# Kernel tuning notes

Hardware: AMD Instinct MI355X
Metric: run time of the kernel (lower is better)

Reference implementation:

```python
import jax, jax.numpy as jnp
import numpy as np

B, N, D_IN, H, D_H, D_OUT = 2, 1024, 1024, 16, 64, 1024
NEG = -1e9


def skew_relative(QE_t):
    # QE_t: [B, H, N, 2N-1] -> [B, H, N, N] via the pad/reshape skew trick
    b, h, n = QE_t.shape[0], QE_t.shape[1], QE_t.shape[2]
    x = jnp.pad(QE_t, ((0, 0), (0, 0), (0, 0), (0, 1)))          # [B,H,N,2N]
    x = x.reshape(b, h, -1)                                       # [B,H,2N^2]
    x = jnp.pad(x, ((0, 0), (0, 0), (0, n - 1)))                  # [B,H,(N+1)(2N-1)]
    x = x.reshape(b, h, n + 1, 2 * n - 1)
    return x[:, :, :n, -n:]


def setup_inputs() -> dict:
    key = jax.random.key(0)
    ks = jax.random.split(key, 8)
    x = jax.random.normal(ks[0], (B, N, D_IN), dtype=jnp.float32)
    E_rel = jax.random.normal(ks[1], (2 * N - 1, D_H), dtype=jnp.float32)
    # additive causal mask [1,1,N,N]
    causal = jnp.tril(jnp.ones((N, N), dtype=bool))
    mask = jnp.where(causal, 0.0, NEG).astype(jnp.float32)[None, None]
    s = 1.0 / np.sqrt(D_IN)
    Wq = jax.random.normal(ks[2], (D_IN, H * D_H), dtype=jnp.float32) * s
    Wk = jax.random.normal(ks[3], (D_IN, H * D_H), dtype=jnp.float32) * s
    Wv = jax.random.normal(ks[4], (D_IN, H * D_H), dtype=jnp.float32) * s
    Wo = jax.random.normal(ks[5], (H * D_H, D_OUT), dtype=jnp.float32) * (1.0 / np.sqrt(H * D_H))
    bo = jnp.zeros((D_OUT,), dtype=jnp.float32)
    return {"x": x, "E_rel": E_rel, "mask": mask, "Wq": Wq, "Wk": Wk, "Wv": Wv, "Wo": Wo, "bo": bo}


def reference(x, E_rel, mask, Wq, Wk, Wv, Wo, bo):
    b = x.shape[0]
    scale = 1.0 / np.sqrt(D_H)
    # project and split heads -> [B, H, N, d]
    Q = (x @ Wq).reshape(b, -1, H, D_H).transpose(0, 2, 1, 3)
    K = (x @ Wk).reshape(b, -1, H, D_H).transpose(0, 2, 1, 3)
    V = (x @ Wv).reshape(b, -1, H, D_H).transpose(0, 2, 1, 3)
    attn = jnp.einsum('bhnd,bhmd->bhnm', Q, K)                    # [B,H,N,N]
    QE_t = jnp.einsum('bhnd,rd->bhnr', Q, E_rel)                  # [B,H,N,2N-1]
    attn = (attn + skew_relative(QE_t)) * scale + mask
    attn = jax.nn.softmax(attn, axis=-1)
    out = jnp.einsum('bhnm,bhmd->bhnd', attn, V)                  # [B,H,N,d]
    out = out.transpose(0, 2, 1, 3).reshape(b, -1, H * D_H)
    return out @ Wo + bo  # dropout is identity at inference
```

## Files before the change

### kernel.cpp

```cpp
#include <hip/hip_runtime.h>
#include <cstdint>
#include <cstddef>

typedef __bf16 bf16;
typedef __bf16 bf16x8 __attribute__((ext_vector_type(8)));
typedef float  f32x4  __attribute__((ext_vector_type(4)));

#define MFMA16(a,b,c) __builtin_amdgcn_mfma_f32_16x16x32_bf16((a),(b),(c),0,0,0)

__device__ __forceinline__ void gload_lds16(const bf16* g, bf16* l) {
  __builtin_amdgcn_global_load_lds((__attribute__((address_space(1))) void*)(g),
                                   (__attribute__((address_space(3))) void*)(l),
                                   16, 0, 0);
}

__global__ __launch_bounds__(256) void prep_k(
    const float* __restrict__ x, const float* __restrict__ E,
    const float* __restrict__ W0, const float* __restrict__ W1,
    const float* __restrict__ W2, const float* __restrict__ W3,
    bf16* __restrict__ xb, bf16* __restrict__ Eb, bf16* __restrict__ Wt) {
  __shared__ float t[32][33];
  const int bid = blockIdx.x;
  const int tid = threadIdx.x;
  if (bid < 2176) {
    const bool isx = (bid < 2048);
    const float* src = isx ? x : E;
    bf16* dst = isx ? xb : Eb;
    const int n = isx ? (2048 * 1024) : (2047 * 64);
    const int i = (isx ? bid : (bid - 2048)) * 1024 + tid * 4;
    if (i < n) {
      float4 v = *(const float4*)(src + i);
      dst[i + 0] = (bf16)v.x;
      dst[i + 1] = (bf16)v.y;
      dst[i + 2] = (bf16)v.z;
      dst[i + 3] = (bf16)v.w;
    }
  } else {
    const int tt = bid - 2176;
    const int z = tt >> 10;
    const int rem = tt & 1023;
    const int cx = (rem & 31) * 32;
    const int ry = (rem >> 5) * 32;
    const float* src = (z == 0) ? W0 : (z == 1) ? W1 : (z == 2) ? W2 : W3;
    bf16* dst = Wt + (size_t)z * (1024 * 1024);
    const int xx = tid & 31, yy = tid >> 5;
    #pragma unroll
    for (int j = 0; j < 32; j += 8) t[yy + j][xx] = src[(size_t)(ry + yy + j) * 1024 + cx + xx];
    __syncthreads();
    #pragma unroll
    for (int j = 0; j < 32; j += 8)
      dst[(size_t)(cx + yy + j) * 1024 + ry + xx] = (bf16)t[xx][yy + j];
  }
}

template <int RM, int RN>
__global__ __launch_bounds__(512, 4) void gemm512(
    const bf16* __restrict__ A, const bf16* __restrict__ Bt,
    bf16* __restrict__ QKV, float* __restrict__ Of,
    const float* __restrict__ bias, const int mode) {
  constexpr int K = 1024;
  constexpr int MT = 2 * RM * 16;
  constexpr int NT = 4 * RN * 16;
  const int row0 = blockIdx.x * MT;
  const int col0 = blockIdx.y * NT;

  __shared__ bf16 As[2][MT * 64];
  __shared__ bf16 Bs[2][NT * 64];

  const int tid = threadIdx.x;
  const int lane = tid & 63;
  const int wid = tid >> 6;
  const int wr = wid >> 2, wc = wid & 3;
  const int lr = lane & 15;
  const int g  = lane >> 4;
  const int srow8 = lane >> 3;
  const int scol = ((lane & 7) ^ srow8) * 8;

  f32x4 acc[RM][RN];
  #pragma unroll
  for (int a = 0; a < RM; ++a)
    #pragma unroll
    for (int b = 0; b < RN; ++b) acc[a][b] = (f32x4){0.f, 0.f, 0.f, 0.f};

  auto stg = [&](int bb, int k0_) {
    constexpr int ARW = MT / 8;
    #pragma unroll
    for (int q = 0; q < ARW / 8; ++q)
      gload_lds16(A + (size_t)(row0 + wid * ARW + q * 8 + srow8) * K + k0_ + scol,
                  &As[bb][(wid * ARW + q * 8) * 64]);
    #pragma unroll
    for (int q = 0; q < 2; ++q)
      gload_lds16(Bt + (size_t)(col0 + wid * 16 + q * 8 + srow8) * K + k0_ + scol,
                  &Bs[bb][(wid * 16 + q * 8) * 64]);
  };

  stg(0, 0);
  for (int t = 0; t < K / 64; ++t) {
    __syncthreads();
    if (t + 1 < K / 64) stg((t + 1) & 1, (t + 1) * 64);
    const bf16* as = &As[t & 1][0];
    const bf16* bs = &Bs[t & 1][0];
    bf16x8 af[RM][2], bfv[RN][2];
    #pragma unroll
    for (int mi = 0; mi < RM; ++mi)
      #pragma unroll
      for (int kk = 0; kk < 2; ++kk)
        af[mi][kk] = *(const bf16x8*)&as[(wr * RM * 16 + mi * 16 + lr) * 64 +
                                         ((kk * 32 + g * 8) ^ ((lr & 7) << 3))];
    #pragma unroll
    for (int ni = 0; ni < RN; ++ni)
      #pragma unroll
      for (int kk = 0; kk < 2; ++kk)
        bfv[ni][kk] = *(const bf16x8*)&bs[(wc * RN * 16 + ni * 16 + lr) * 64 +
                                          ((kk * 32 + g * 8) ^ ((lr & 7) << 3))];
    #pragma unroll
    for (int mi = 0; mi < RM; ++mi)
      #pragma unroll
      for (int ni = 0; ni < RN; ++ni)
        #pragma unroll
        for (int kk = 0; kk < 2; ++kk)
          acc[mi][ni] = MFMA16(af[mi][kk], bfv[ni][kk], acc[mi][ni]);
  }

  #pragma unroll
  for (int mi = 0; mi < RM; ++mi) {
    #pragma unroll
    for (int ni = 0; ni < RN; ++ni) {
      #pragma unroll
      for (int r = 0; r < 4; ++r) {
        const int row = row0 + wr * RM * 16 + mi * 16 + g * 4 + r;
        const int col = col0 + wc * RN * 16 + ni * 16 + lr;
        const float v = acc[mi][ni][r];
        if (mode == 2) {
          Of[(size_t)row * 1024 + col] = v + bias[col];
        } else {
          const int b = row >> 10, i = row & 1023;
          const int which = col >> 10, cc = col & 1023;
          const int h = cc >> 6, d = cc & 63;
          if (which < 2)
            QKV[(size_t)which * 2097152 + (((size_t)(b * 16 + h)) * 1024 + i) * 64 + d] = (bf16)v;
          else
            QKV[(size_t)2 * 2097152 + (((size_t)(b * 16 + h)) * 64 + d) * 1024 + i] = (bf16)v;
        }
      }
    }
  }
}

__device__ const int CH_QB[36] = {7,7,7,7,7,7,7, 6,6,6,6,6,6, 5,5,5,5,5, 4,4,4,4,
                                  3,3,3, 2,2, 1, 0,1,2,3,4,5,6,7};
__device__ const int CH_K0[36] = {0,2,4,6,8,10,12, 0,2,4,6,8,10, 0,2,4,6,8, 0,2,4,6,
                                  0,2,4, 0,2, 0, 0,2,4,6,8,10,12,14};
__device__ const int QB_P0[8] = {0,1,3,6,10,15,21,28};

__global__ __launch_bounds__(512, 4) void attn_kernel(
    const bf16* __restrict__ Qh, const bf16* __restrict__ Kh,
    const bf16* __restrict__ Vt, const bf16* __restrict__ Eb,
    bf16* __restrict__ OP, float* __restrict__ LP) {
  constexpr int N = 1024;
  const int flat = blockIdx.y * 36 + blockIdx.x;
  const int task = (flat & 7) * 144 + (flat >> 3);
  const int bh = task / 36;
  const int ch = task - bh * 36;
  const int qb = CH_QB[ch];
  const int kb0 = CH_K0[ch];
  const int i0 = qb * 128;

  const bf16* Qp = Qh + (size_t)bh * N * 64;
  const bf16* Kp = Kh + (size_t)bh * N * 64;
  const bf16* Vp = Vt + (size_t)bh * 64 * N;

  __shared__ bf16 Ks[2][64 * 64];
  __shared__ bf16 Vs[2][64 * 64];
  __shared__ bf16 Es[256 * 64];
  __shared__ bf16 Psm[8][16 * 64];

  const int tid = threadIdx.x;
  const int lane = tid & 63;
  const int wid = tid >> 6;
  const int lr = lane & 15;
  const int g  = lane >> 4;
  const int iw0 = i0 + wid * 16;
  bf16* pp = &Psm[wid][0];

  const int srow8 = lane >> 3;
  const int sch = ((lane & 7) ^ srow8) * 8;

  bf16x8 qf[2];
  {
    const bf16* qrow = Qp + (size_t)(iw0 + lr) * 64 + g * 8;
    qf[0] = *(const bf16x8*)(qrow);
    qf[1] = *(const bf16x8*)(qrow + 32);
  }

  float lb[4] = {0.f, 0.f, 0.f, 0.f};
  f32x4 oacc[4];
  #pragma unroll
  for (int r = 0; r < 4; ++r) oacc[r] = (f32x4){0.f, 0.f, 0.f, 0.f};

  constexpr float SC = 0.18033688f;
  const int fb = 7 - wid;
  const int j0a = kb0 * 64;
  const int ebase0 = (N - 128) + j0a - i0;

  auto STAGE_KV = [&](int b, int j0) {
    gload_lds16(Kp + (size_t)(j0 + wid * 8 + srow8) * 64 + sch, &Ks[b][(wid * 8) * 64]);
    gload_lds16(Vp + (size_t)(wid * 8 + srow8) * 1024 + j0 + sch, &Vs[b][(wid * 8) * 64]);
  };
  auto STAGE_E = [&]() {
    #pragma unroll
    for (int q = 0; q < 4; ++q)
      gload_lds16(Eb + (size_t)(ebase0 + wid * 32 + q * 8 + srow8) * 64 + sch,
                  &Es[(wid * 32 + q * 8) * 64]);
  };

  auto TILE = [&](int buf, int j0, int eoff) {
    if (j0 > iw0 + 15) return;
    const bf16* kbuf = &Ks[buf][0];
    const bf16* vbuf = &Vs[buf][0];
    f32x4 sa[4];
    #pragma unroll
    for (int ni = 0; ni < 4; ++ni) sa[ni] = (f32x4){0.f, 0.f, 0.f, 0.f};
    __builtin_amdgcn_s_setprio(1);
    #pragma unroll
    for (int ni = 0; ni < 4; ++ni)
      #pragma unroll
      for (int kk = 0; kk < 2; ++kk) {
        bf16x8 kf = *(const bf16x8*)&kbuf[(ni * 16 + lr) * 64 +
                                          ((kk * 32 + g * 8) ^ ((lr & 7) << 3))];
        sa[ni] = MFMA16(qf[kk], kf, sa[ni]);
      }
    f32x4 ea[5];
    #pragma unroll
    for (int s5 = 0; s5 < 5; ++s5) {
      const int er = eoff + (fb + s5) * 16 + lr;
      ea[s5] = (f32x4){0.f, 0.f, 0.f, 0.f};
      bf16x8 e0 = *(const bf16x8*)&Es[er * 64 + ((g * 8) ^ ((lr & 7) << 3))];
      bf16x8 e1 = *(const bf16x8*)&Es[er * 64 + ((32 + g * 8) ^ ((lr & 7) << 3))];
      ea[s5] = MFMA16(qf[0], e0, ea[s5]);
      ea[s5] = MFMA16(qf[1], e1, ea[s5]);
    }
    __builtin_amdgcn_s_setprio(0);
    #pragma unroll
    for (int r = 0; r < 4; ++r) {
      const int di = g * 4 + r;
      const int sl = (g << 4) | ((lr - di - 1) & 15);
      const float sh0 = __shfl(ea[0][r], sl);
      const float sh1 = __shfl(ea[1][r], sl);
      const float sh2 = __shfl(ea[2][r], sl);
      const float sh3 = __shfl(ea[3][r], sl);
      const float sh4 = __shfl(ea[4][r], sl);
      const bool hi = (lr > di);
      const float rel[4] = {hi ? sh1 : sh0, hi ? sh2 : sh1, hi ? sh3 : sh2, hi ? sh4 : sh3};
      const int ig = iw0 + di;
      #pragma unroll
      for (int ni = 0; ni < 4; ++ni) {
        float tv = (sa[ni][r] + rel[ni]) * SC;
        tv = (j0 + ni * 16 + lr > ig) ? -1e30f : tv;
        const float pv = exp2f(tv);
        lb[r] += pv;
        pp[di * 64 + ((ni * 16 + lr) ^ ((di & 7) << 3))] = (bf16)pv;
      }
    }
    bf16x8 pf[2];
    pf[0] = *(const bf16x8*)&pp[lr * 64 + ((g * 8) ^ ((lr & 7) << 3))];
    pf[1] = *(const bf16x8*)&pp[lr * 64 + ((32 + g * 8) ^ ((lr & 7) << 3))];
    __builtin_amdgcn_s_setprio(1);
    #pragma unroll
    for (int nd = 0; nd < 4; ++nd)
      #pragma unroll
      for (int kk = 0; kk < 2; ++kk) {
        bf16x8 vf = *(const bf16x8*)&vbuf[(nd * 16 + lr) * 64 +
                                          ((kk * 32 + g * 8) ^ ((lr & 7) << 3))];
        oacc[nd] = MFMA16(pf[kk], vf, oacc[nd]);
      }
    __builtin_amdgcn_s_setprio(0);
  };

  STAGE_E();
  STAGE_KV(0, j0a);
  __syncthreads();
  STAGE_KV(1, j0a + 64);
  TILE(0, j0a, 0);
  __syncthreads();
  TILE(1, j0a + 64, 64);

  #pragma unroll
  for (int off = 1; off < 16; off <<= 1)
    #pragma unroll
    for (int r = 0; r < 4; ++r)
      lb[r] += __shfl_xor(lb[r], off);

  const int pslot = bh * 36 + QB_P0[qb] + (kb0 >> 1);
  bf16* Op = OP + (size_t)pslot * 8192;
  #pragma unroll
  for (int nd = 0; nd < 4; ++nd)
    #pragma unroll
    for (int r = 0; r < 4; ++r)
      Op[(size_t)(wid * 16 + g * 4 + r) * 64 + nd * 16 + lr] = (bf16)oacc[nd][r];
  if (lr == 0) {
    #pragma unroll
    for (int r = 0; r < 4; ++r)
      LP[pslot * 128 + wid * 16 + g * 4 + r] = lb[r];
  }
}

__global__ __launch_bounds__(256) void merge_k(const bf16* __restrict__ OP,
                                               const float* __restrict__ LP,
                                               bf16* __restrict__ AO) {
  const int bh = blockIdx.x;
  const int qb = blockIdx.y;
  const int half = blockIdx.z;
  const int np = qb + 1;
  const int tid = threadIdx.x;
  const int row = half * 64 + (tid >> 2);
  const int c0 = (tid & 3) * 16;
  const int p0 = bh * 36 + QB_P0[qb];

  float o[16];
  #pragma unroll
  for (int j = 0; j < 16; ++j) o[j] = 0.f;
  float l = 0.f;
  for (int c = 0; c < np; ++c) {
    l += LP[(p0 + c) * 128 + row];
    const bf16* Oc = OP + (size_t)(p0 + c) * 8192 + row * 64 + c0;
    #pragma unroll
    for (int j = 0; j < 16; j += 8) {
      const bf16x8 v = *(const bf16x8*)&Oc[j];
      #pragma unroll
      for (int u = 0; u < 8; ++u) o[j + u] += (float)v[u];
    }
  }
  const float inv = 1.f / l;

  const int b = bh >> 4, h = bh & 15;
  bf16* dst = AO + ((size_t)(b * 1024) + qb * 128 + row) * 1024 + h * 64 + c0;
  #pragma unroll
  for (int j = 0; j < 16; ++j) dst[j] = (bf16)(o[j] * inv);
}

extern "C" void kernel_launch(void* const* d_in, const int* in_sizes, int n_in,
                              void* d_out, int out_size, void* d_ws, size_t ws_size,
                              hipStream_t stream) {
  const float* x  = (const float*)d_in[0];
  const float* E  = (const float*)d_in[1];
  const float* Wq = (const float*)d_in[3];
  const float* Wk = (const float*)d_in[4];
  const float* Wv = (const float*)d_in[5];
  const float* Wo = (const float*)d_in[6];
  const float* bo = (const float*)d_in[7];

  bf16* xb  = (bf16*)d_ws;
  bf16* Wqt = xb + 2048 * 1024;
  bf16* Wot = Wqt + 3 * 1024 * 1024;
  bf16* Eb  = Wqt + 4 * 1024 * 1024;
  bf16* Qh  = Eb + 2048 * 64;
  bf16* AO  = Qh + 3 * 2048 * 1024;
  bf16* OPb = AO + 2048 * 1024;
  float* LPp = (float*)(OPb + (size_t)1152 * 8192);
  float* out = (float*)d_out;

  prep_k<<<dim3(6272), dim3(256), 0, stream>>>(x, E, Wq, Wk, Wv, Wo, xb, Eb, Wqt);

  gemm512<4, 2><<<dim3(16, 24), dim3(512), 0, stream>>>(xb, Wqt, Qh, nullptr, nullptr, 0);

  attn_kernel<<<dim3(36, 32), dim3(512), 0, stream>>>(
      Qh, Qh + 2048 * 1024, Qh + 2 * 2048 * 1024, Eb, OPb, LPp);

  merge_k<<<dim3(32, 8, 2), dim3(256), 0, stream>>>(OPb, LPp, AO);

  gemm512<2, 2><<<dim3(32, 8), dim3(512), 0, stream>>>(AO, Wot, nullptr, out, bo, 2);
}
```

Before: 83.77 us.

## Fuse split-KV partial merge into output projection GEMM A-tile loading

Removes the separate merge kernel and the intermediate AO buffer by having the output projection GEMM build its A tiles directly from the partial attention outputs and row sums, normalising on the fly. The GEMM is specialised into a new kernel with its own load path, and the QKV GEMM loses its mode branch. This saves one launch and an AO write/read round trip, but each of the 8 column blocks now re-reads and re-reduces the partials for its rows. The A load is a blocking register path rather than async LDS loads, which may expose latency.

```diff
diff --git a/kernel.cpp b/kernel.cpp
--- a/kernel.cpp
+++ b/kernel.cpp
@@ -56,16 +56,14 @@
 template <int RM, int RN>
 __global__ __launch_bounds__(512, 4) void gemm512(
     const bf16* __restrict__ A, const bf16* __restrict__ Bt,
-    bf16* __restrict__ QKV, float* __restrict__ Of,
-    const float* __restrict__ bias, const int mode) {
+    bf16* __restrict__ QKV) {
   constexpr int K = 1024;
   constexpr int MT = 2 * RM * 16;
-  constexpr int NT = 4 * RN * 16;
   const int row0 = blockIdx.x * MT;
-  const int col0 = blockIdx.y * NT;
+  const int col0 = blockIdx.y * 128;
 
   __shared__ bf16 As[2][MT * 64];
-  __shared__ bf16 Bs[2][NT * 64];
+  __shared__ bf16 Bs[2][128 * 64];
 
   const int tid = threadIdx.x;
   const int lane = tid & 63;
@@ -131,17 +129,13 @@
         const int row = row0 + wr * RM * 16 + mi * 16 + g * 4 + r;
         const int col = col0 + wc * RN * 16 + ni * 16 + lr;
         const float v = acc[mi][ni][r];
-        if (mode == 2) {
-          Of[(size_t)row * 1024 + col] = v + bias[col];
-        } else {
-          const int b = row >> 10, i = row & 1023;
-          const int which = col >> 10, cc = col & 1023;
-          const int h = cc >> 6, d = cc & 63;
-          if (which < 2)
-            QKV[(size_t)which * 2097152 + (((size_t)(b * 16 + h)) * 1024 + i) * 64 + d] = (bf16)v;
-          else
-            QKV[(size_t)2 * 2097152 + (((size_t)(b * 16 + h)) * 64 + d) * 1024 + i] = (bf16)v;
-        }
+        const int b = row >> 10, i = row & 1023;
+        const int which = col >> 10, cc = col & 1023;
+        const int h = cc >> 6, d = cc & 63;
+        if (which < 2)
+          QKV[(size_t)which * 2097152 + (((size_t)(b * 16 + h)) * 1024 + i) * 64 + d] = (bf16)v;
+        else
+          QKV[(size_t)2 * 2097152 + (((size_t)(b * 16 + h)) * 64 + d) * 1024 + i] = (bf16)v;
       }
     }
   }
@@ -305,38 +299,112 @@
   }
 }
 
-__global__ __launch_bounds__(256) void merge_k(const bf16* __restrict__ OP,
-                                               const float* __restrict__ LP,
-                                               bf16* __restrict__ AO) {
-  const int bh = blockIdx.x;
-  const int qb = blockIdx.y;
-  const int half = blockIdx.z;
+__global__ __launch_bounds__(512, 2) void outproj_k(
+    const bf16* __restrict__ OP, const float* __restrict__ LP,
+    const bf16* __restrict__ Bt, float* __restrict__ Of,
+    const float* __restrict__ bias) {
+  constexpr int K = 1024;
+  const int row0 = blockIdx.x * 64;
+  const int col0 = blockIdx.y * 128;
+
+  __shared__ bf16 As[2][64 * 64];
+  __shared__ bf16 Bs[2][128 * 64];
+
+  const int tid = threadIdx.x;
+  const int lane = tid & 63;
+  const int wid = tid >> 6;
+  const int wr = wid >> 2, wc = wid & 3;
+  const int lr = lane & 15;
+  const int g  = lane >> 4;
+  const int srow8 = lane >> 3;
+  const int scol = ((lane & 7) ^ srow8) * 8;
+
+  const int ar = wid * 8 + srow8;
+  const int gr = row0 + ar;
+  const int b  = gr >> 10;
+  const int i  = gr & 1023;
+  const int qb = i >> 7;
+  const int lrow = i & 127;
   const int np = qb + 1;
-  const int tid = threadIdx.x;
-  const int row = half * 64 + (tid >> 2);
-  const int c0 = (tid & 3) * 16;
-  const int p0 = bh * 36 + QB_P0[qb];
-
-  float o[16];
-  #pragma unroll
-  for (int j = 0; j < 16; ++j) o[j] = 0.f;
-  float l = 0.f;
-  for (int c = 0; c < np; ++c) {
-    l += LP[(p0 + c) * 128 + row];
-    const bf16* Oc = OP + (size_t)(p0 + c) * 8192 + row * 64 + c0;
-    #pragma unroll
-    for (int j = 0; j < 16; j += 8) {
-      const bf16x8 v = *(const bf16x8*)&Oc[j];
-      #pragma unroll
-      for (int u = 0; u < 8; ++u) o[j + u] += (float)v[u];
+  const int p0base = QB_P0[qb];
+  const int d0 = scol;
+  bf16* adst[2] = {&As[0][ar * 64 + (lane & 7) * 8], &As[1][ar * 64 + (lane & 7) * 8]};
+
+  float av[8];
+  float lsum;
+  auto ldA = [&](int t) {
+    const int p0 = (b * 16 + t) * 36 + p0base;
+    lsum = 0.f;
+    #pragma unroll
+    for (int j = 0; j < 8; ++j) av[j] = 0.f;
+    for (int c = 0; c < np; ++c) {
+      lsum += LP[(p0 + c) * 128 + lrow];
+      const bf16x8 v = *(const bf16x8*)&OP[(size_t)(p0 + c) * 8192 + lrow * 64 + d0];
+      #pragma unroll
+      for (int j = 0; j < 8; ++j) av[j] += (float)v[j];
     }
-  }
-  const float inv = 1.f / l;
-
-  const int b = bh >> 4, h = bh & 15;
-  bf16* dst = AO + ((size_t)(b * 1024) + qb * 128 + row) * 1024 + h * 64 + c0;
-  #pragma unroll
-  for (int j = 0; j < 16; ++j) dst[j] = (bf16)(o[j] * inv);
+  };
+  auto wA = [&](int bb) {
+    const float inv = 1.f / lsum;
+    bf16x8 o;
+    #pragma unroll
+    for (int j = 0; j < 8; ++j) o[j] = (bf16)(av[j] * inv);
+    *(bf16x8*)adst[bb] = o;
+  };
+  auto gB = [&](int bb, int k0_) {
+    #pragma unroll
+    for (int q = 0; q < 2; ++q)
+      gload_lds16(Bt + (size_t)(col0 + wid * 16 + q * 8 + srow8) * K + k0_ + scol,
+                  &Bs[bb][(wid * 16 + q * 8) * 64]);
+  };
+
+  f32x4 acc[2][2];
+  #pragma unroll
+  for (int a = 0; a < 2; ++a)
+    #pragma unroll
+    for (int bb = 0; bb < 2; ++bb) acc[a][bb] = (f32x4){0.f, 0.f, 0.f, 0.f};
+
+  ldA(0);
+  gB(0, 0);
+  wA(0);
+  for (int t = 0; t < 16; ++t) {
+    __syncthreads();
+    if (t + 1 < 16) { ldA(t + 1); gB((t + 1) & 1, (t + 1) * 64); }
+    const bf16* as = &As[t & 1][0];
+    const bf16* bs = &Bs[t & 1][0];
+    bf16x8 af[2][2], bfv[2][2];
+    #pragma unroll
+    for (int mi = 0; mi < 2; ++mi)
+      #pragma unroll
+      for (int kk = 0; kk < 2; ++kk)
+        af[mi][kk] = *(const bf16x8*)&as[(wr * 32 + mi * 16 + lr) * 64 +
+                                         ((kk * 32 + g * 8) ^ ((lr & 7) << 3))];
+    #pragma unroll
+    for (int ni = 0; ni < 2; ++ni)
+      #pragma unroll
+      for (int kk = 0; kk < 2; ++kk)
+        bfv[ni][kk] = *(const bf16x8*)&bs[(wc * 32 + ni * 16 + lr) * 64 +
+                                          ((kk * 32 + g * 8) ^ ((lr & 7) << 3))];
+    #pragma unroll
+    for (int mi = 0; mi < 2; ++mi)
+      #pragma unroll
+      for (int ni = 0; ni < 2; ++ni)
+        #pragma unroll
+        for (int kk = 0; kk < 2; ++kk)
+          acc[mi][ni] = MFMA16(af[mi][kk], bfv[ni][kk], acc[mi][ni]);
+    if (t + 1 < 16) wA((t + 1) & 1);
+  }
+
+  #pragma unroll
+  for (int mi = 0; mi < 2; ++mi)
+    #pragma unroll
+    for (int ni = 0; ni < 2; ++ni)
+      #pragma unroll
+      for (int r = 0; r < 4; ++r) {
+        const int row = row0 + wr * 32 + mi * 16 + g * 4 + r;
+        const int col = col0 + wc * 32 + ni * 16 + lr;
+        Of[(size_t)row * 1024 + col] = acc[mi][ni][r] + bias[col];
+      }
 }
 
 extern "C" void kernel_launch(void* const* d_in, const int* in_sizes, int n_in,
@@ -355,19 +423,16 @@
   bf16* Wot = Wqt + 3 * 1024 * 1024;
   bf16* Eb  = Wqt + 4 * 1024 * 1024;
   bf16* Qh  = Eb + 2048 * 64;
-  bf16* AO  = Qh + 3 * 2048 * 1024;
-  bf16* OPb = AO + 2048 * 1024;
+  bf16* OPb = Qh + 3 * 2048 * 1024;
   float* LPp = (float*)(OPb + (size_t)1152 * 8192);
   float* out = (float*)d_out;
 
   prep_k<<<dim3(6272), dim3(256), 0, stream>>>(x, E, Wq, Wk, Wv, Wo, xb, Eb, Wqt);
 
-  gemm512<4, 2><<<dim3(16, 24), dim3(512), 0, stream>>>(xb, Wqt, Qh, nullptr, nullptr, 0);
+  gemm512<4, 2><<<dim3(16, 24), dim3(512), 0, stream>>>(xb, Wqt, Qh);
 
   attn_kernel<<<dim3(36, 32), dim3(512), 0, stream>>>(
       Qh, Qh + 2048 * 1024, Qh + 2 * 2048 * 1024, Eb, OPb, LPp);
 
-  merge_k<<<dim3(32, 8, 2), dim3(256), 0, stream>>>(OPb, LPp, AO);
-
-  gemm512<2, 2><<<dim3(32, 8), dim3(512), 0, stream>>>(AO, Wot, nullptr, out, bo, 2);
-}
+  outproj_k<<<dim3(32, 8), dim3(512), 0, stream>>>(OPb, LPp, Wot, out, bo);
+}
```

Measured after the change: 105.6 us. +26.0%, slower.
